# Kernel tuning notes

Measured on AMD Instinct MI355X. Metric: run time of the kernel, lower is better.

The kernel has to match this reference:

```python
import jax, jax.numpy as jnp
import numpy as np

B, S, D = 4, 2048, 1024
N_EXPERTS, EXPERT_SIZE = 16, 256
WIDTH = N_EXPERTS * EXPERT_SIZE  # 4096


def setup_inputs() -> dict:
    key = jax.random.key(0)
    k_x, k_w1, k_w2, k_g = jax.random.split(key, 4)
    x = jax.random.normal(k_x, (B, S, D), dtype=jnp.float32)
    # Linear params, fan-in scaled init
    w1 = jax.random.normal(k_w1, (D, WIDTH), dtype=jnp.float32) / np.sqrt(D).astype(np.float32)
    b1 = jnp.zeros((WIDTH,), dtype=jnp.float32)
    w2 = jax.random.normal(k_w2, (WIDTH, D), dtype=jnp.float32) / np.sqrt(WIDTH).astype(np.float32)
    b2 = jnp.zeros((D,), dtype=jnp.float32)
    return {"x": x, "w1": w1, "b1": b1, "w2": w2, "b2": b2}


def reference(x, w1, b1, w2, b2):
    # NOTE: the original module computes expert-choice routing tensors
    # (gate einsum -> topk -> one_hot -> identity matmul 'gather'), but the
    # returned value is ONLY the dense FFN applied to x; all routing results
    # are dead code with no effect on the output. Faithful output math:
    h = jax.nn.relu(jnp.einsum('bsd,dw->bsw', x, w1) + b1)  # [B,S,WIDTH]
    return jnp.einsum('bsw,wd->bsd', h, w2) + b2            # [B,S,D]
```

## Files before the change

kernel.cpp:

```cpp
#include <hip/hip_runtime.h>
#include <hip/hip_bf16.h>


typedef __bf16 bf16;
typedef __bf16 bf16x4 __attribute__((ext_vector_type(4)));
typedef __bf16 bf16x8 __attribute__((ext_vector_type(8)));
typedef float  f32x4  __attribute__((ext_vector_type(4)));

#define BM 128
#define BN 128
#define BK 64

__device__ __forceinline__ void gload_lds16(const bf16* g, bf16* l) {
    __builtin_amdgcn_global_load_lds(
        (const __attribute__((address_space(1))) unsigned int*)g,
        (__attribute__((address_space(3))) unsigned int*)l,
        16, 0, 0);
}

__device__ __forceinline__ void transpose_tile(
    const float* __restrict__ in, bf16* __restrict__ out,
    int K, int N, int bx, int by, int t, bf16 (*tile)[72])
{
    const int k0 = by * 64;
    const int n0 = bx * 64;
    const int lr = t >> 4;
    const int lc = (t & 15) << 2;
#pragma unroll
    for (int p = 0; p < 4; ++p) {
        int k = p * 16 + lr;
        float4 v = *(const float4*)(in + (size_t)(k0 + k) * N + n0 + lc);
        tile[lc + 0][k] = (bf16)v.x;
        tile[lc + 1][k] = (bf16)v.y;
        tile[lc + 2][k] = (bf16)v.z;
        tile[lc + 3][k] = (bf16)v.w;
    }
    __syncthreads();
    const int wr = t >> 3;
    const int wc = (t & 7) << 3;
#pragma unroll
    for (int p = 0; p < 2; ++p) {
        int n = p * 32 + wr;
        *(bf16x8*)(out + (size_t)(n0 + n) * K + k0 + wc) =
            *(const bf16x8*)&tile[n][wc];
    }
}

__global__ __launch_bounds__(256) void prep(
    const float* __restrict__ x,  bf16* __restrict__ xb,
    const float* __restrict__ w1, bf16* __restrict__ w1t,
    const float* __restrict__ w2, bf16* __restrict__ w2t)
{
    __shared__ __align__(16) bf16 tile[64][72];
    const int b = blockIdx.x;
    const int t = threadIdx.x;
    if (b < 8192) {
        int i = b * 256 + t;
        float4 v = ((const float4*)x)[i];
        bf16x4 o;
        o.x = (bf16)v.x; o.y = (bf16)v.y; o.z = (bf16)v.z; o.w = (bf16)v.w;
        ((bf16x4*)xb)[i] = o;
    } else if (b < 9216) {
        int b2 = b - 8192;
        transpose_tile(w1, w1t, 1024, 4096, b2 & 63, b2 >> 6, t, tile);
    } else {
        int b2 = b - 9216;
        transpose_tile(w2, w2t, 4096, 1024, b2 & 15, b2 >> 4, t, tile);
    }
}

template <int FUSE_RELU_BF16>
__global__ __launch_bounds__(256, 2) void gemm_bt(
    const bf16* __restrict__ A, const bf16* __restrict__ Bt,
    const float* __restrict__ bias, void* __restrict__ Cout,
    int M, int N, int K, int nx)
{
    __shared__ __align__(16) bf16 As[2][BM * BK];
    __shared__ __align__(16) bf16 Bs[2][BN * BK];

    const int lid = blockIdx.x;
    const int xcd = lid & 7;
    const int j   = lid >> 3;
    const int bx  = j % nx;
    const int by  = (j / nx) * 8 + xcd;

    const int tid  = threadIdx.x;
    const int wave = tid >> 6;
    const int lane = tid & 63;

    const int l8  = lane >> 3;
    const int c8  = lane & 7;
    const int swc = (c8 ^ l8) << 3;
    const size_t K_ = (size_t)K;

    const bf16* gA[4]; const bf16* gB[4];
#pragma unroll
    for (int g = 0; g < 4; ++g) {
        const int rr = wave * 32 + g * 8 + l8;
        gA[g] = A  + ((size_t)by * BM + rr) * K_ + swc;
        gB[g] = Bt + ((size_t)bx * BN + rr) * K_ + swc;
    }
    const int lofs = (wave * 32) * BK + lane * 8;

    const int wm   = (wave >> 1) << 6;
    const int wn   = (wave & 1) << 6;
    const int quad = lane >> 4;
    const int r    = lane & 15;
    const int r7   = lane & 7;

    f32x4 acc[4][4] = {};

    auto stage = [&](int buf) {
#pragma unroll
        for (int g = 0; g < 4; ++g) {
            gload_lds16(gA[g], &As[buf][lofs + g * (8 * BK)]);
            gload_lds16(gB[g], &Bs[buf][lofs + g * (8 * BK)]);
            gA[g] += BK; gB[g] += BK;
        }
    };
    auto compute = [&](int buf) {
#pragma unroll
        for (int h = 0; h < 2; ++h) {
            const int ch = ((h * 4 + quad) ^ r7) << 3;
            bf16x8 af[4], bfr[4];
#pragma unroll
            for (int i = 0; i < 4; ++i)
                af[i] = *(const bf16x8*)&As[buf][(wm + i * 16 + r) * BK + ch];
#pragma unroll
            for (int jj = 0; jj < 4; ++jj)
                bfr[jj] = *(const bf16x8*)&Bs[buf][(wn + jj * 16 + r) * BK + ch];
#pragma unroll
            for (int i = 0; i < 4; ++i)
#pragma unroll
                for (int jj = 0; jj < 4; ++jj)
                    acc[i][jj] = __builtin_amdgcn_mfma_f32_16x16x32_bf16(
                        af[i], bfr[jj], acc[i][jj], 0, 0, 0);
        }
    };

    const int T = K / BK;
    stage(0);
    for (int t = 0; t < T; t += 2) {
        __syncthreads();
        stage(1);
        compute(0);
        __syncthreads();
        if (t + 2 < T) stage(0);
        compute(1);
    }

    const int m_base = by * BM + wm + quad * 4;
    const int n_base = bx * BN + wn + r;
    float bv[4];
#pragma unroll
    for (int jj = 0; jj < 4; ++jj) bv[jj] = bias[n_base + jj * 16];

    if (FUSE_RELU_BF16) {
        bf16* Cb = (bf16*)Cout;
#pragma unroll
        for (int i = 0; i < 4; ++i) {
#pragma unroll
            for (int p = 0; p < 4; ++p) {
                size_t row = (size_t)(m_base + i * 16 + p) * (size_t)N;
#pragma unroll
                for (int jj = 0; jj < 4; ++jj) {
                    float v = acc[i][jj][p] + bv[jj];
                    v = v > 0.f ? v : 0.f;
                    Cb[row + n_base + jj * 16] = (bf16)v;
                }
            }
        }
    } else {
        float* Cf = (float*)Cout;
#pragma unroll
        for (int i = 0; i < 4; ++i) {
#pragma unroll
            for (int p = 0; p < 4; ++p) {
                size_t row = (size_t)(m_base + i * 16 + p) * (size_t)N;
#pragma unroll
                for (int jj = 0; jj < 4; ++jj) {
                    Cf[row + n_base + jj * 16] = acc[i][jj][p] + bv[jj];
                }
            }
        }
    }
}

extern "C" void kernel_launch(void* const* d_in, const int* in_sizes, int n_in,
                              void* d_out, int out_size, void* d_ws, size_t ws_size,
                              hipStream_t stream)
{
    const float* x  = (const float*)d_in[0];
    const float* w1 = (const float*)d_in[1];
    const float* b1 = (const float*)d_in[2];
    const float* w2 = (const float*)d_in[3];
    const float* b2 = (const float*)d_in[4];
    float* out = (float*)d_out;

    const int M = 8192, D = 1024, W = 4096;

    char* ws = (char*)d_ws;
    bf16* xb  = (bf16*)(ws);
    bf16* w1t = (bf16*)(ws + (size_t)(16 << 20));
    bf16* w2t = (bf16*)(ws + (size_t)(24 << 20));
    bf16* h   = (bf16*)(ws + (size_t)(32 << 20));

    prep<<<8192 + 1024 + 1024, 256, 0, stream>>>(x, xb, w1, w1t, w2, w2t);

    gemm_bt<1><<<(W / BN) * (M / BM), 256, 0, stream>>>(
        xb, w1t, b1, (void*)h, M, W, D, W / BN);

    gemm_bt<0><<<(D / BN) * (M / BM), 256, 0, stream>>>(
        h, w2t, b2, (void*)out, M, D, W, D / BN);
}
```

Baseline: 268.0 us.

## Enlarge GEMM M-tile to 256 and drop LDS double buffering

Doubles the block tile along M to 256 rows, so each wave now computes a 128x64 output sub-tile (8x4 MFMA accumulators) and reuses each loaded B fragment across twice as many MFMAs. To fit LDS, it removes the double-buffered staging and uses a single buffer with a sync before and after each load. The larger tile raises arithmetic intensity per LDS and global byte. In exchange, global-to-LDS loads no longer overlap with compute, and the doubled accumulator set raises register pressure, which may lower occupancy below the two blocks requested by the launch bounds.

```diff
diff --git a/kernel.cpp b/kernel.cpp
--- a/kernel.cpp
+++ b/kernel.cpp
@@ -7,7 +7,7 @@
 typedef __bf16 bf16x8 __attribute__((ext_vector_type(8)));
 typedef float  f32x4  __attribute__((ext_vector_type(4)));
 
-#define BM 128
+#define BM 256
 #define BN 128
 #define BK 64
 
@@ -75,8 +75,8 @@
     const float* __restrict__ bias, void* __restrict__ Cout,
     int M, int N, int K, int nx)
 {
-    __shared__ __align__(16) bf16 As[2][BM * BK];
-    __shared__ __align__(16) bf16 Bs[2][BN * BK];
+    __shared__ __align__(16) bf16 As[BM * BK];
+    __shared__ __align__(16) bf16 Bs[BN * BK];
 
     const int lid = blockIdx.x;
     const int xcd = lid & 7;
@@ -93,60 +93,54 @@
     const int swc = (c8 ^ l8) << 3;
     const size_t K_ = (size_t)K;
 
-    const bf16* gA[4]; const bf16* gB[4];
-#pragma unroll
-    for (int g = 0; g < 4; ++g) {
-        const int rr = wave * 32 + g * 8 + l8;
-        gA[g] = A  + ((size_t)by * BM + rr) * K_ + swc;
-        gB[g] = Bt + ((size_t)bx * BN + rr) * K_ + swc;
-    }
-    const int lofs = (wave * 32) * BK + lane * 8;
-
-    const int wm   = (wave >> 1) << 6;
+    const bf16* gA[8]; const bf16* gB[4];
+#pragma unroll
+    for (int g = 0; g < 8; ++g)
+        gA[g] = A + ((size_t)by * BM + wave * 64 + g * 8 + l8) * K_ + swc;
+#pragma unroll
+    for (int g = 0; g < 4; ++g)
+        gB[g] = Bt + ((size_t)bx * BN + wave * 32 + g * 8 + l8) * K_ + swc;
+    bf16* lA0 = &As[(wave * 64) * BK] + lane * 8;
+    bf16* lB0 = &Bs[(wave * 32) * BK] + lane * 8;
+
+    const int wm   = (wave >> 1) << 7;
     const int wn   = (wave & 1) << 6;
     const int quad = lane >> 4;
     const int r    = lane & 15;
     const int r7   = lane & 7;
 
-    f32x4 acc[4][4] = {};
-
-    auto stage = [&](int buf) {
+    f32x4 acc[8][4] = {};
+
+    for (int k0 = 0; k0 < K; k0 += BK) {
+        __syncthreads();
+#pragma unroll
+        for (int g = 0; g < 8; ++g) {
+            gload_lds16(gA[g], lA0 + g * (8 * BK));
+            gA[g] += BK;
+        }
 #pragma unroll
         for (int g = 0; g < 4; ++g) {
-            gload_lds16(gA[g], &As[buf][lofs + g * (8 * BK)]);
-            gload_lds16(gB[g], &Bs[buf][lofs + g * (8 * BK)]);
-            gA[g] += BK; gB[g] += BK;
-        }
-    };
-    auto compute = [&](int buf) {
+            gload_lds16(gB[g], lB0 + g * (8 * BK));
+            gB[g] += BK;
+        }
+        __syncthreads();
+
 #pragma unroll
         for (int h = 0; h < 2; ++h) {
             const int ch = ((h * 4 + quad) ^ r7) << 3;
-            bf16x8 af[4], bfr[4];
-#pragma unroll
-            for (int i = 0; i < 4; ++i)
-                af[i] = *(const bf16x8*)&As[buf][(wm + i * 16 + r) * BK + ch];
+            bf16x8 bfr[4];
 #pragma unroll
             for (int jj = 0; jj < 4; ++jj)
-                bfr[jj] = *(const bf16x8*)&Bs[buf][(wn + jj * 16 + r) * BK + ch];
-#pragma unroll
-            for (int i = 0; i < 4; ++i)
+                bfr[jj] = *(const bf16x8*)&Bs[(wn + jj * 16 + r) * BK + ch];
+#pragma unroll
+            for (int i = 0; i < 8; ++i) {
+                bf16x8 af = *(const bf16x8*)&As[(wm + i * 16 + r) * BK + ch];
 #pragma unroll
                 for (int jj = 0; jj < 4; ++jj)
                     acc[i][jj] = __builtin_amdgcn_mfma_f32_16x16x32_bf16(
-                        af[i], bfr[jj], acc[i][jj], 0, 0, 0);
-        }
-    };
-
-    const int T = K / BK;
-    stage(0);
-    for (int t = 0; t < T; t += 2) {
-        __syncthreads();
-        stage(1);
-        compute(0);
-        __syncthreads();
-        if (t + 2 < T) stage(0);
-        compute(1);
+                        af, bfr[jj], acc[i][jj], 0, 0, 0);
+            }
+        }
     }
 
     const int m_base = by * BM + wm + quad * 4;
@@ -158,7 +152,7 @@
     if (FUSE_RELU_BF16) {
         bf16* Cb = (bf16*)Cout;
 #pragma unroll
-        for (int i = 0; i < 4; ++i) {
+        for (int i = 0; i < 8; ++i) {
 #pragma unroll
             for (int p = 0; p < 4; ++p) {
                 size_t row = (size_t)(m_base + i * 16 + p) * (size_t)N;
@@ -173,7 +167,7 @@
     } else {
         float* Cf = (float*)Cout;
 #pragma unroll
-        for (int i = 0; i < 4; ++i) {
+        for (int i = 0; i < 8; ++i) {
 #pragma unroll
             for (int p = 0; p < 4; ++p) {
                 size_t row = (size_t)(m_base + i * 16 + p) * (size_t)N;
```

After: 263.6 us. About the same (-1.7%).

## Replace double-buffered LDS DMA loads with register-staged single-buffer pipeline

Applied to the files above, without the earlier changes.

Drops the direct global-to-LDS loads and the double-buffered shared tiles. Each tile is now loaded into registers, written to a single LDS buffer with an XOR swizzle, and the next tile's global load is issued before the MFMA compute. Halving LDS use, together with raising launch bounds to 3 blocks per CU, is meant to increase occupancy and hide latency. In exchange it adds register pressure and an extra LDS write pass, and leaves two barriers per K step.

```diff
diff --git a/kernel.cpp b/kernel.cpp
--- a/kernel.cpp
+++ b/kernel.cpp
@@ -10,13 +10,6 @@
 #define BM 128
 #define BN 128
 #define BK 64
-
-__device__ __forceinline__ void gload_lds16(const bf16* g, bf16* l) {
-    __builtin_amdgcn_global_load_lds(
-        (const __attribute__((address_space(1))) unsigned int*)g,
-        (__attribute__((address_space(3))) unsigned int*)l,
-        16, 0, 0);
-}
 
 __device__ __forceinline__ void transpose_tile(
     const float* __restrict__ in, bf16* __restrict__ out,
@@ -70,13 +63,13 @@
 }
 
 template <int FUSE_RELU_BF16>
-__global__ __launch_bounds__(256, 2) void gemm_bt(
+__global__ __launch_bounds__(256, 3) void gemm_bt(
     const bf16* __restrict__ A, const bf16* __restrict__ Bt,
     const float* __restrict__ bias, void* __restrict__ Cout,
     int M, int N, int K, int nx)
 {
-    __shared__ __align__(16) bf16 As[2][BM * BK];
-    __shared__ __align__(16) bf16 Bs[2][BN * BK];
+    __shared__ __align__(16) bf16 As[BM * BK];
+    __shared__ __align__(16) bf16 Bs[BN * BK];
 
     const int lid = blockIdx.x;
     const int xcd = lid & 7;
@@ -90,17 +83,12 @@
 
     const int l8  = lane >> 3;
     const int c8  = lane & 7;
-    const int swc = (c8 ^ l8) << 3;
     const size_t K_ = (size_t)K;
-
-    const bf16* gA[4]; const bf16* gB[4];
-#pragma unroll
-    for (int g = 0; g < 4; ++g) {
-        const int rr = wave * 32 + g * 8 + l8;
-        gA[g] = A  + ((size_t)by * BM + rr) * K_ + swc;
-        gB[g] = Bt + ((size_t)bx * BN + rr) * K_ + swc;
-    }
-    const int lofs = (wave * 32) * BK + lane * 8;
+    const size_t g8 = 8 * K_;
+
+    const bf16* pA = A  + ((size_t)by * BM + wave * 32 + l8) * K_ + c8 * 8;
+    const bf16* pB = Bt + ((size_t)bx * BN + wave * 32 + l8) * K_ + c8 * 8;
+    const int wofs = (wave * 32 + l8) * BK + ((c8 ^ l8) << 3);
 
     const int wm   = (wave >> 1) << 6;
     const int wn   = (wave & 1) << 6;
@@ -109,26 +97,34 @@
     const int r7   = lane & 7;
 
     f32x4 acc[4][4] = {};
-
-    auto stage = [&](int buf) {
+    bf16x8 rA[4], rB[4];
+
+    auto gload = [&]() {
 #pragma unroll
         for (int g = 0; g < 4; ++g) {
-            gload_lds16(gA[g], &As[buf][lofs + g * (8 * BK)]);
-            gload_lds16(gB[g], &Bs[buf][lofs + g * (8 * BK)]);
-            gA[g] += BK; gB[g] += BK;
-        }
+            rA[g] = *(const bf16x8*)(pA + g * g8);
+            rB[g] = *(const bf16x8*)(pB + g * g8);
+        }
+        pA += BK; pB += BK;
     };
-    auto compute = [&](int buf) {
+    auto lwrite = [&]() {
+#pragma unroll
+        for (int g = 0; g < 4; ++g) {
+            *(bf16x8*)&As[wofs + g * (8 * BK)] = rA[g];
+            *(bf16x8*)&Bs[wofs + g * (8 * BK)] = rB[g];
+        }
+    };
+    auto compute = [&]() {
 #pragma unroll
         for (int h = 0; h < 2; ++h) {
             const int ch = ((h * 4 + quad) ^ r7) << 3;
             bf16x8 af[4], bfr[4];
 #pragma unroll
             for (int i = 0; i < 4; ++i)
-                af[i] = *(const bf16x8*)&As[buf][(wm + i * 16 + r) * BK + ch];
+                af[i] = *(const bf16x8*)&As[(wm + i * 16 + r) * BK + ch];
 #pragma unroll
             for (int jj = 0; jj < 4; ++jj)
-                bfr[jj] = *(const bf16x8*)&Bs[buf][(wn + jj * 16 + r) * BK + ch];
+                bfr[jj] = *(const bf16x8*)&Bs[(wn + jj * 16 + r) * BK + ch];
 #pragma unroll
             for (int i = 0; i < 4; ++i)
 #pragma unroll
@@ -139,14 +135,13 @@
     };
 
     const int T = K / BK;
-    stage(0);
-    for (int t = 0; t < T; t += 2) {
+    gload();
+    for (int t = 0; t < T; ++t) {
         __syncthreads();
-        stage(1);
-        compute(0);
+        lwrite();
         __syncthreads();
-        if (t + 2 < T) stage(0);
-        compute(1);
+        if (t + 1 < T) gload();
+        compute();
     }
 
     const int m_base = by * BM + wm + quad * 4;
```

New measurement: 264.8 us. About the same (-1.2%).

## Pre-pack weights in MFMA fragment order and load B straight into registers

Applied to the files above, without the earlier changes.

The prep kernel now writes the transposed bf16 weights in a layout that matches the 16x16x32 MFMA B-operand fragments. The GEMM then loads B directly from global memory into a double-buffered register set instead of staging it through LDS, which removes the B LDS buffers and their LDS reads. K and N become template constants, and the block-index swizzle is hardcoded for 64 row tiles. In exchange, waves that share the same N half load the same B data twice from cache, and holding B in registers raises VGPR pressure and leaves global-load latency covered only by a one-step prefetch.

```diff
diff --git a/kernel.cpp b/kernel.cpp
--- a/kernel.cpp
+++ b/kernel.cpp
@@ -18,7 +18,7 @@
         16, 0, 0);
 }
 
-__device__ __forceinline__ void transpose_tile(
+__device__ __forceinline__ void transpose_tile_frag(
     const float* __restrict__ in, bf16* __restrict__ out,
     int K, int N, int bx, int by, int t, bf16 (*tile)[72])
 {
@@ -36,13 +36,17 @@
         tile[lc + 3][k] = (bf16)v.w;
     }
     __syncthreads();
+    const int KC = K >> 5;
     const int wr = t >> 3;
     const int wc = (t & 7) << 3;
 #pragma unroll
     for (int p = 0; p < 2; ++p) {
         int n = p * 32 + wr;
-        *(bf16x8*)(out + (size_t)(n0 + n) * K + k0 + wc) =
-            *(const bf16x8*)&tile[n][wc];
+        int gn = n0 + n, gk = k0 + wc;
+        int f = gn >> 4, r = gn & 15;
+        int c = gk >> 5, quad = (gk >> 3) & 3;
+        size_t off = ((size_t)((f * KC + c) * 64 + quad * 16 + r)) << 3;
+        *(bf16x8*)(out + off) = *(const bf16x8*)&tile[n][wc];
     }
 }
 
@@ -62,45 +66,40 @@
         ((bf16x4*)xb)[i] = o;
     } else if (b < 9216) {
         int b2 = b - 8192;
-        transpose_tile(w1, w1t, 1024, 4096, b2 & 63, b2 >> 6, t, tile);
+        transpose_tile_frag(w1, w1t, 1024, 4096, b2 & 63, b2 >> 6, t, tile);
     } else {
         int b2 = b - 9216;
-        transpose_tile(w2, w2t, 4096, 1024, b2 & 15, b2 >> 4, t, tile);
-    }
-}
-
-template <int FUSE_RELU_BF16>
+        transpose_tile_frag(w2, w2t, 4096, 1024, b2 & 15, b2 >> 4, t, tile);
+    }
+}
+
+template <int FUSE_RELU_BF16, int K, int N>
 __global__ __launch_bounds__(256, 2) void gemm_bt(
-    const bf16* __restrict__ A, const bf16* __restrict__ Bt,
-    const float* __restrict__ bias, void* __restrict__ Cout,
-    int M, int N, int K, int nx)
-{
+    const bf16* __restrict__ A, const bf16* __restrict__ Bf,
+    const float* __restrict__ bias, void* __restrict__ Cout)
+{
+    constexpr int KC = K >> 5;
+    constexpr int T  = K / BK;
     __shared__ __align__(16) bf16 As[2][BM * BK];
-    __shared__ __align__(16) bf16 Bs[2][BN * BK];
 
     const int lid = blockIdx.x;
     const int xcd = lid & 7;
-    const int j   = lid >> 3;
-    const int bx  = j % nx;
-    const int by  = (j / nx) * 8 + xcd;
+    const int i2  = lid >> 3;
+    const int bx  = i2 >> 3;
+    const int by  = (i2 & 7) * 8 + xcd;
 
     const int tid  = threadIdx.x;
     const int wave = tid >> 6;
     const int lane = tid & 63;
 
-    const int l8  = lane >> 3;
-    const int c8  = lane & 7;
+    const int l8 = lane >> 3;
+    const int c8 = lane & 7;
     const int swc = (c8 ^ l8) << 3;
-    const size_t K_ = (size_t)K;
-
-    const bf16* gA[4]; const bf16* gB[4];
-#pragma unroll
-    for (int g = 0; g < 4; ++g) {
-        const int rr = wave * 32 + g * 8 + l8;
-        gA[g] = A  + ((size_t)by * BM + rr) * K_ + swc;
-        gB[g] = Bt + ((size_t)bx * BN + rr) * K_ + swc;
-    }
-    const int lofs = (wave * 32) * BK + lane * 8;
+    const bf16* gA[4];
+#pragma unroll
+    for (int g = 0; g < 4; ++g)
+        gA[g] = A + ((size_t)by * BM + wave * 32 + g * 8 + l8) * K + swc;
+    const int lofsA = (wave * 32) * BK + lane * 8;
 
     const int wm   = (wave >> 1) << 6;
     const int wn   = (wave & 1) << 6;
@@ -108,45 +107,56 @@
     const int r    = lane & 15;
     const int r7   = lane & 7;
 
-    f32x4 acc[4][4] = {};
-
-    auto stage = [&](int buf) {
+    const int f0 = bx * 8 + (wave & 1) * 4;
+    const bf16* pB = Bf + (size_t)f0 * KC * 512 + lane * 8;
+
+    f32x4  acc[4][4] = {};
+    bf16x8 rB[2][8];
+
+    auto stageA = [&](int lb) {
 #pragma unroll
         for (int g = 0; g < 4; ++g) {
-            gload_lds16(gA[g], &As[buf][lofs + g * (8 * BK)]);
-            gload_lds16(gB[g], &Bs[buf][lofs + g * (8 * BK)]);
-            gA[g] += BK; gB[g] += BK;
+            gload_lds16(gA[g], &As[lb][lofsA + g * (8 * BK)]);
+            gA[g] += BK;
         }
     };
-    auto compute = [&](int buf) {
+    auto prefB = [&](int set) {
+#pragma unroll
+        for (int jj = 0; jj < 4; ++jj)
+#pragma unroll
+            for (int h = 0; h < 2; ++h)
+                rB[set][jj * 2 + h] =
+                    *(const bf16x8*)(pB + ((size_t)jj * KC + h) * 512);
+        pB += 1024;
+    };
+    auto compute = [&](int lb, int set) {
 #pragma unroll
         for (int h = 0; h < 2; ++h) {
             const int ch = ((h * 4 + quad) ^ r7) << 3;
-            bf16x8 af[4], bfr[4];
+            bf16x8 af[4];
 #pragma unroll
             for (int i = 0; i < 4; ++i)
-                af[i] = *(const bf16x8*)&As[buf][(wm + i * 16 + r) * BK + ch];
-#pragma unroll
-            for (int jj = 0; jj < 4; ++jj)
-                bfr[jj] = *(const bf16x8*)&Bs[buf][(wn + jj * 16 + r) * BK + ch];
+                af[i] = *(const bf16x8*)&As[lb][(wm + i * 16 + r) * BK + ch];
 #pragma unroll
             for (int i = 0; i < 4; ++i)
 #pragma unroll
                 for (int jj = 0; jj < 4; ++jj)
                     acc[i][jj] = __builtin_amdgcn_mfma_f32_16x16x32_bf16(
-                        af[i], bfr[jj], acc[i][jj], 0, 0, 0);
+                        af[i], rB[set][jj * 2 + h], acc[i][jj], 0, 0, 0);
         }
     };
 
-    const int T = K / BK;
-    stage(0);
+    stageA(0);
+    prefB(0);
+    __syncthreads();
     for (int t = 0; t < T; t += 2) {
+        stageA(1);
+        prefB(1);
+        compute(0, 0);
         __syncthreads();
-        stage(1);
-        compute(0);
+        if (t + 2 < T) { stageA(0); prefB(0); }
+        compute(1, 1);
         __syncthreads();
-        if (t + 2 < T) stage(0);
-        compute(1);
     }
 
     const int m_base = by * BM + wm + quad * 4;
@@ -207,9 +217,9 @@
 
     prep<<<8192 + 1024 + 1024, 256, 0, stream>>>(x, xb, w1, w1t, w2, w2t);
 
-    gemm_bt<1><<<(W / BN) * (M / BM), 256, 0, stream>>>(
-        xb, w1t, b1, (void*)h, M, W, D, W / BN);
-
-    gemm_bt<0><<<(D / BN) * (M / BM), 256, 0, stream>>>(
-        h, w2t, b2, (void*)out, M, D, W, D / BN);
-}
+    gemm_bt<1, 1024, 4096><<<(W / BN) * (M / BM), 256, 0, stream>>>(
+        xb, w1t, b1, (void*)h);
+
+    gemm_bt<0, 4096, 1024><<<(D / BN) * (M / BM), 256, 0, stream>>>(
+        h, w2t, b2, (void*)out);
+}
```

Result: slower. 280.2 us (+4.5%).
